# Kernel tuning notes

Measured on AMD Instinct MI355X. Metric: run time of the kernel, lower is better.

The kernel has to match this reference:

```python
import jax, jax.numpy as jnp
import numpy as np

B, S, H, L, NH, FF, V, T = 32, 512, 768, 6, 12, 3072, 30522, 7
DH = H // NH


def setup_inputs():
    key = jax.random.key(0)
    ks = iter(jax.random.split(key, 32))

    def w(shape, scale=0.02):
        return jax.random.normal(next(ks), shape, jnp.float32) * scale

    inp = {
        "word_emb": w((V, H)),
        "pos_emb": w((S, H)),
        "emb_ln_s": jnp.ones((H,), jnp.float32),
        "emb_ln_b": jnp.zeros((H,), jnp.float32),
        "attn_qw": w((L, H, H)), "attn_qb": jnp.zeros((L, H), jnp.float32),
        "attn_kw": w((L, H, H)), "attn_kb": jnp.zeros((L, H), jnp.float32),
        "attn_vw": w((L, H, H)), "attn_vb": jnp.zeros((L, H), jnp.float32),
        "attn_ow": w((L, H, H)), "attn_ob": jnp.zeros((L, H), jnp.float32),
        "ln1_s": jnp.ones((L, H), jnp.float32), "ln1_b": jnp.zeros((L, H), jnp.float32),
        "ffn_w1": w((L, H, FF)), "ffn_b1": jnp.zeros((L, FF), jnp.float32),
        "ffn_w2": w((L, FF, H)), "ffn_b2": jnp.zeros((L, H), jnp.float32),
        "ln2_s": jnp.ones((L, H), jnp.float32), "ln2_b": jnp.zeros((L, H), jnp.float32),
        "cls_w": w((H, T)), "cls_b": jnp.zeros((T,), jnp.float32),
        "crf_start": w((T,), 0.1), "crf_end": w((T,), 0.1), "crf_trans": w((T, T), 0.1),
    }
    lengths = jax.random.randint(next(ks), (B,), S // 2, S + 1)
    attention_mask = (jnp.arange(S)[None, :] < lengths[:, None]).astype(jnp.int32)
    raw_labels = jax.random.randint(next(ks), (B, S), 0, T)
    inp["input_ids"] = jax.random.randint(next(ks), (B, S), 0, V)
    inp["attention_mask"] = attention_mask
    inp["labels"] = jnp.where(attention_mask == 1, raw_labels, -100)  # -100 = ignore
    return inp


def _layer_norm(x, s, b, eps=1e-12):
    m = x.mean(-1, keepdims=True)
    v = ((x - m) ** 2).mean(-1, keepdims=True)
    return (x - m) / jnp.sqrt(v + eps) * s + b


def _forward(params, input_ids, attention_mask, labels):
    (word_emb, pos_emb, emb_ln_s, emb_ln_b, attn_qw, attn_qb, attn_kw, attn_kb,
     attn_vw, attn_vb, attn_ow, attn_ob, ln1_s, ln1_b, ffn_w1, ffn_b1, ffn_w2,
     ffn_b2, ln2_s, ln2_b, cls_w, cls_b, crf_start, crf_end, crf_trans) = params
    amask = attention_mask.astype(bool)            # [B,S]
    # DistilBERT embeddings (word + position, then LayerNorm; dropout = identity in eval)
    x = word_emb[input_ids] + pos_emb[None, :, :]  # [B,S,H]
    x = _layer_norm(x, emb_ln_s, emb_ln_b)
    neg = jnp.finfo(x.dtype).min
    for i in range(L):  # 6 structurally distinct transformer layers
        q = (x @ attn_qw[i] + attn_qb[i]).reshape(B, S, NH, DH).transpose(0, 2, 1, 3)
        k = (x @ attn_kw[i] + attn_kb[i]).reshape(B, S, NH, DH).transpose(0, 2, 1, 3)
        v = (x @ attn_vw[i] + attn_vb[i]).reshape(B, S, NH, DH).transpose(0, 2, 1, 3)
        scores = jnp.einsum('bhqd,bhkd->bhqk', q, k) / jnp.sqrt(jnp.float32(DH))
        scores = jnp.where(amask[:, None, None, :], scores, neg)
        probs = jax.nn.softmax(scores, axis=-1)
        ctx = jnp.einsum('bhqk,bhkd->bhqd', probs, v).transpose(0, 2, 1, 3).reshape(B, S, H)
        x = _layer_norm(x + ctx @ attn_ow[i] + attn_ob[i], ln1_s[i], ln1_b[i])
        h = jax.nn.gelu(x @ ffn_w1[i] + ffn_b1[i], approximate=False)
        x = _layer_norm(x + h @ ffn_w2[i] + ffn_b2[i], ln2_s[i], ln2_b[i])
    emissions = x @ cls_w + cls_b                  # [B,S,T]

    # ---- CRF negative mean log-likelihood (torchcrf semantics, batch_first) ----
    mask = (labels != -100).at[:, 0].set(True)     # [B,S] bool
    safe = jnp.where(mask, labels, 0)
    safe = safe.at[:, 0].set(jnp.clip(safe[:, 0], 0, T - 1))
    b_idx = jnp.arange(B)
    # numerator: score of the given tag sequence
    emit = jnp.take_along_axis(emissions, safe[:, :, None], axis=2)[:, :, 0]  # [B,S]
    trans = crf_trans[safe[:, :-1], safe[:, 1:]]                              # [B,S-1]
    num = crf_start[safe[:, 0]] + emit[:, 0]
    num = num + jnp.sum(jnp.where(mask[:, 1:], trans + emit[:, 1:], 0.0), axis=1)
    seq_ends = mask.sum(axis=1) - 1
    num = num + crf_end[safe[b_idx, seq_ends]]
    # denominator: forward algorithm (logsumexp recursion over timesteps)
    alpha0 = crf_start[None, :] + emissions[:, 0]  # [B,T]

    def step(alpha, xs):
        em_t, m_t = xs                              # [B,T], [B]
        nxt = jax.nn.logsumexp(alpha[:, :, None] + crf_trans[None] + em_t[:, None, :], axis=1)
        return jnp.where(m_t[:, None], nxt, alpha), None

    alpha, _ = jax.lax.scan(step, alpha0,
                            (emissions[:, 1:].transpose(1, 0, 2), mask[:, 1:].T))
    denom = jax.nn.logsumexp(alpha + crf_end[None, :], axis=1)
    return -(num - denom).mean()  # reduction='mean', returned negated


def reference(word_emb, pos_emb, emb_ln_s, emb_ln_b, attn_qw, attn_qb, attn_kw,
              attn_kb, attn_vw, attn_vb, attn_ow, attn_ob, ln1_s, ln1_b, ffn_w1,
              ffn_b1, ffn_w2, ffn_b2, ln2_s, ln2_b, cls_w, cls_b, crf_start,
              crf_end, crf_trans, input_ids, attention_mask, labels):
    params = (word_emb, pos_emb, emb_ln_s, emb_ln_b, attn_qw, attn_qb, attn_kw,
              attn_kb, attn_vw, attn_vb, attn_ow, attn_ob, ln1_s, ln1_b, ffn_w1,
              ffn_b1, ffn_w2, ffn_b2, ln2_s, ln2_b, cls_w, cls_b, crf_start,
              crf_end, crf_trans)
    return _forward(params, input_ids, attention_mask, labels)
```

## Files before the change

kernel.cpp:

```cpp
#include <hip/hip_runtime.h>

constexpr int cB = 32, cS = 512, cH = 768, cL = 6, cNH = 12, cFF = 3072, cT = 7;
constexpr int cM = cB * cS;
constexpr int cDH = cH / cNH;
constexpr int cQS = 2304;

#define DEVI __device__ __forceinline__

typedef __attribute__((ext_vector_type(8))) short bh8_t;
typedef __attribute__((ext_vector_type(4))) float f4_t;
typedef __attribute__((ext_vector_type(4))) unsigned short us4_t;

DEVI unsigned short f2bf(float f) {
  unsigned int u = __float_as_uint(f);
  return (unsigned short)((u + 0x7fffu + ((u >> 16) & 1u)) >> 16);
}
DEVI float bf2f(unsigned short h) { return __uint_as_float(((unsigned int)h) << 16); }

DEVI float fast_erff(float x) {
  const float a = fabsf(x);
  const float t = 1.0f / (1.0f + 0.3275911f * a);
  const float y = 1.0f - (((((1.061405429f * t - 1.453152027f) * t) + 1.421413741f) * t
                            - 0.284496736f) * t + 0.254829592f) * t * __expf(-a * a);
  return copysignf(y, x);
}

typedef __attribute__((address_space(1))) void* gas_t;
typedef __attribute__((address_space(3))) void* las_t;
DEVI void async16(void* lds, const void* g) {
  __builtin_amdgcn_global_load_lds((gas_t)g, (las_t)lds, 16, 0, 0);
}

struct WtransArgs { const float* src[6]; };

__global__ void wtrans_all(WtransArgs args, unsigned short* __restrict__ out) {
  const int m = blockIdx.z;
  const int K = (m == 5) ? cFF : cH;
  const int N = (m == 4) ? cFF : cH;
  int n0, k0;
  if (m < 4) {
    if (blockIdx.x >= 24) return;
    n0 = blockIdx.x * 32; k0 = blockIdx.y * 32;
  } else if (m == 4) {
    n0 = blockIdx.x * 32; k0 = blockIdx.y * 32;
  } else {
    k0 = blockIdx.x * 32; n0 = blockIdx.y * 32;
  }
  const int woffs[6] = {0, 589824, 1179648, 1769472, 2359296, 4718592};
  const float* in = args.src[m];
  unsigned short* o = out + woffs[m];
  __shared__ float tile[32][33];
  const int tx = threadIdx.x, ty = threadIdx.y;
#pragma unroll
  for (int i = 0; i < 4; i++)
    tile[ty + i * 8][tx] = in[(size_t)(k0 + ty + i * 8) * N + n0 + tx];
  __syncthreads();
#pragma unroll
  for (int i = 0; i < 4; i++)
    o[(size_t)(n0 + ty + i * 8) * K + k0 + tx] = f2bf(tile[tx][ty + i * 8]);
}

__global__ void concat_bias(const float* __restrict__ qb, const float* __restrict__ kb,
                            const float* __restrict__ vb, float* __restrict__ out) {
  const int c = blockIdx.x * 256 + threadIdx.x;
  if (c < cQS)
    out[c] = c < cH ? qb[c] : (c < 2 * cH ? kb[c - cH] : vb[c - 2 * cH]);
}

template <bool RESID, bool GELU, bool OUTB>
__global__ __launch_bounds__(256) void gemm_bf16(
    const unsigned short* __restrict__ A, const unsigned short* __restrict__ Bt,
    const float* __restrict__ bias, const float* resid,
    float* outf, unsigned short* __restrict__ outb, int N, int K) {
  __shared__ __align__(16) unsigned short As[128 * 32];
  __shared__ __align__(16) unsigned short Bs[128 * 32];
  const int tid = threadIdx.x;
  const int lane = tid & 63;
  const int wave = tid >> 6;
  const int wm = wave >> 1, wn = wave & 1;
  const int quad = lane >> 4, col = lane & 15;
  const int m0 = blockIdx.y * 128;
  const int n0 = blockIdx.x * 128;

  f4_t acc[4][4] = {};

  const int rA = tid >> 2;
  const int cXor = ((tid & 3) ^ ((tid >> 3) & 3)) << 3;
  const unsigned short* gA = A + (size_t)(m0 + rA) * K + cXor;
  const unsigned short* gB = Bt + (size_t)(n0 + rA) * K + cXor;
  unsigned short* lA0 = As + wave * 512;
  unsigned short* lA1 = As + 2048 + wave * 512;
  unsigned short* lB0 = Bs + wave * 512;
  unsigned short* lB1 = Bs + 2048 + wave * 512;

  const int physq = quad ^ ((col >> 1) & 3);
  const unsigned short* fA[4];
  const unsigned short* fB[4];
#pragma unroll
  for (int t = 0; t < 4; t++) {
    fA[t] = As + (size_t)(wm * 64 + t * 16 + col) * 32 + physq * 8;
    fB[t] = Bs + (size_t)(wn * 64 + t * 16 + col) * 32 + physq * 8;
  }

  for (int k0 = 0; k0 < K; k0 += 32) {
    async16(lA0, gA + k0);
    async16(lA1, gA + (size_t)64 * K + k0);
    async16(lB0, gB + k0);
    async16(lB1, gB + (size_t)64 * K + k0);
    __syncthreads();
    bh8_t af[4], bf[4];
#pragma unroll
    for (int t = 0; t < 4; t++) af[t] = *(const bh8_t*)fA[t];
#pragma unroll
    for (int t = 0; t < 4; t++) bf[t] = *(const bh8_t*)fB[t];
#pragma unroll
    for (int mi = 0; mi < 4; mi++)
#pragma unroll
      for (int ni = 0; ni < 4; ni++)
        acc[mi][ni] = __builtin_amdgcn_mfma_f32_16x16x32_bf16(bf[ni], af[mi],
                                                              acc[mi][ni], 0, 0, 0);
    __syncthreads();
  }

#pragma unroll
  for (int mi = 0; mi < 4; mi++) {
    const size_t rowbase = (size_t)(m0 + wm * 64 + mi * 16 + col) * N;
#pragma unroll
    for (int ni = 0; ni < 4; ni++) {
      const int cb = n0 + wn * 64 + ni * 16 + quad * 4;
      f4_t v = acc[mi][ni] + *(const f4_t*)(bias + cb);
      if (RESID) v += *(const f4_t*)(resid + rowbase + cb);
      if (GELU) {
#pragma unroll
        for (int r = 0; r < 4; r++)
          v[r] = 0.5f * v[r] * (1.0f + fast_erff(v[r] * 0.70710678118654752f));
      }
      if (OUTB) {
        us4_t u;
#pragma unroll
        for (int r = 0; r < 4; r++) u[r] = f2bf(v[r]);
        *(us4_t*)(outb + rowbase + cb) = u;
      } else {
        *(f4_t*)(outf + rowbase + cb) = v;
      }
    }
  }
}

__global__ __launch_bounds__(256) void embed_ln(
    const int* __restrict__ ids, const float* __restrict__ wemb,
    const float* __restrict__ pemb, const float* __restrict__ g,
    const float* __restrict__ be, float* __restrict__ xo,
    unsigned short* __restrict__ xbo) {
  const int token = blockIdx.x;
  const int tid = threadIdx.x;
  const int id = ids[token];
  const int pos = token & (cS - 1);
  const float* wr = wemb + (size_t)id * cH;
  const float* pr = pemb + (size_t)pos * cH;
  float v[3];
#pragma unroll
  for (int i = 0; i < 3; i++) v[i] = wr[tid + i * 256] + pr[tid + i * 256];
  float s = v[0] + v[1] + v[2];
  float s2 = v[0] * v[0] + v[1] * v[1] + v[2] * v[2];
#pragma unroll
  for (int off = 32; off; off >>= 1) { s += __shfl_xor(s, off); s2 += __shfl_xor(s2, off); }
  __shared__ float sa[4], sb[4];
  if ((tid & 63) == 0) { sa[tid >> 6] = s; sb[tid >> 6] = s2; }
  __syncthreads();
  s = sa[0] + sa[1] + sa[2] + sa[3];
  s2 = sb[0] + sb[1] + sb[2] + sb[3];
  const float mean = s * (1.0f / cH);
  const float rstd = rsqrtf(s2 * (1.0f / cH) - mean * mean + 1e-12f);
  float* xr = xo + (size_t)token * cH;
  unsigned short* xbr = xbo + (size_t)token * cH;
#pragma unroll
  for (int i = 0; i < 3; i++) {
    const int c = tid + i * 256;
    const float nv = (v[i] - mean) * rstd * g[c] + be[c];
    xr[c] = nv;
    xbr[c] = f2bf(nv);
  }
}

__global__ __launch_bounds__(256) void ln_fused(
    float* __restrict__ x, const float* __restrict__ g,
    const float* __restrict__ be, unsigned short* __restrict__ xbo) {
  const int token = blockIdx.x;
  const int tid = threadIdx.x;
  float* row = x + (size_t)token * cH;
  float v[3];
#pragma unroll
  for (int i = 0; i < 3; i++) v[i] = row[tid + i * 256];
  float s = v[0] + v[1] + v[2];
  float s2 = v[0] * v[0] + v[1] * v[1] + v[2] * v[2];
#pragma unroll
  for (int off = 32; off; off >>= 1) { s += __shfl_xor(s, off); s2 += __shfl_xor(s2, off); }
  __shared__ float sa[4], sb[4];
  if ((tid & 63) == 0) { sa[tid >> 6] = s; sb[tid >> 6] = s2; }
  __syncthreads();
  s = sa[0] + sa[1] + sa[2] + sa[3];
  s2 = sb[0] + sb[1] + sb[2] + sb[3];
  const float mean = s * (1.0f / cH);
  const float rstd = rsqrtf(s2 * (1.0f / cH) - mean * mean + 1e-12f);
  unsigned short* xbr = xbo + (size_t)token * cH;
#pragma unroll
  for (int i = 0; i < 3; i++) {
    const int c = tid + i * 256;
    const float nv = (v[i] - mean) * rstd * g[c] + be[c];
    row[c] = nv;
    xbr[c] = f2bf(nv);
  }
}

__global__ __launch_bounds__(256, 2) void attn_mfma(
    const unsigned short* __restrict__ qkv, const int* __restrict__ amask,
    unsigned short* __restrict__ ctxb) {
  __shared__ __align__(16) unsigned short Ks[128 * 64];
  __shared__ __align__(16) unsigned short Vt[64 * 128];
  __shared__ __align__(16) unsigned short Ps[4 * 32 * 136];
  __shared__ int lensh[4];

  const int tid = threadIdx.x, lane = tid & 63, wave = tid >> 6;
  const int quad = lane >> 4, col = lane & 15;
  const int wg = blockIdx.x;
  const int qb = wg & 3, h = (wg >> 2) % cNH, b = wg / (4 * cNH);
  const int q0 = qb * 128 + wave * 32;

  const unsigned short* qg = qkv;
  const unsigned short* kg = qkv + cH;
  const unsigned short* vg = qkv + 2 * cH;

  const int* mrow = amask + b * cS;
  int c = mrow[tid] + mrow[tid + 256];
#pragma unroll
  for (int off = 32; off; off >>= 1) c += __shfl_xor(c, off);
  if (lane == 0) lensh[wave] = c;
  __syncthreads();
  const int len = lensh[0] + lensh[1] + lensh[2] + lensh[3];

  const unsigned short* qbase = qg + (size_t)(b * cS + q0) * cQS + h * cDH;
  bh8_t qf[2][2];
#pragma unroll
  for (int mi = 0; mi < 2; mi++)
#pragma unroll
    for (int ks = 0; ks < 2; ks++)
      qf[mi][ks] = *(const bh8_t*)(qbase + (size_t)(mi * 16 + col) * cQS + ks * 32 + quad * 8);

  float mr[2][4], lr[2][4];
  f4_t o[2][4] = {};
#pragma unroll
  for (int mi = 0; mi < 2; mi++)
#pragma unroll
    for (int r = 0; r < 4; r++) { mr[mi][r] = -3.0e38f; lr[mi][r] = 0.0f; }

  unsigned short* Pw = Ps + wave * (32 * 136);

  for (int k0 = 0; k0 < cS; k0 += 128) {
    if (k0 >= len) break;
    __syncthreads();
    const unsigned short* kb = kg + (size_t)(b * cS + k0) * cQS + h * cDH;
    const unsigned short* vb = vg + (size_t)(b * cS + k0) * cQS + h * cDH;
#pragma unroll
    for (int i = 0; i < 4; i++) {
      const int chunk = i * 256 + tid;
      const int key = chunk >> 3;
      const int ld = (chunk & 7) ^ (key & 7);
      async16(Ks + (size_t)(i * 256 + wave * 64) * 8, kb + (size_t)key * cQS + ld * 8);
    }
#pragma unroll
    for (int i = 0; i < 4; i++) {
      const int chunk = i * 256 + tid;
      const int key = chunk >> 3;
      const int ld = chunk & 7;
      const int bk = key >> 3;
      bh8_t vv = *(const bh8_t*)(vb + (size_t)key * cQS + ld * 8);
      unsigned short vs[8];
      *(bh8_t*)vs = vv;
#pragma unroll
      for (int j = 0; j < 8; j++) {
        const int d = ld * 8 + j;
        const int pb = bk ^ j ^ ld;
        Vt[d * 128 + pb * 8 + (key & 7)] = vs[j];
      }
    }
    __syncthreads();

    f4_t s[2][8];
#pragma unroll
    for (int mi = 0; mi < 2; mi++)
#pragma unroll
      for (int n = 0; n < 8; n++) s[mi][n] = f4_t{0.f, 0.f, 0.f, 0.f};
#pragma unroll
    for (int n = 0; n < 8; n++) {
      const int r = n * 16 + col;
#pragma unroll
      for (int ks = 0; ks < 2; ks++) {
        const int phys = (ks * 4 + quad) ^ (col & 7);
        bh8_t kf = *(const bh8_t*)(Ks + (size_t)r * 64 + phys * 8);
        s[0][n] = __builtin_amdgcn_mfma_f32_16x16x32_bf16(qf[0][ks], kf, s[0][n], 0, 0, 0);
        s[1][n] = __builtin_amdgcn_mfma_f32_16x16x32_bf16(qf[1][ks], kf, s[1][n], 0, 0, 0);
      }
    }
#pragma unroll
    for (int n = 0; n < 8; n++) {
      const bool valid = (k0 + n * 16 + col) < len;
#pragma unroll
      for (int mi = 0; mi < 2; mi++)
#pragma unroll
        for (int r = 0; r < 4; r++)
          s[mi][n][r] = valid ? s[mi][n][r] * 0.125f : -3.0e38f;
    }
#pragma unroll
    for (int mi = 0; mi < 2; mi++)
#pragma unroll
      for (int r = 0; r < 4; r++) {
        float v = s[mi][0][r];
#pragma unroll
        for (int n = 1; n < 8; n++) v = fmaxf(v, s[mi][n][r]);
#pragma unroll
        for (int off = 1; off < 16; off <<= 1) v = fmaxf(v, __shfl_xor(v, off));
        const float nm = fmaxf(mr[mi][r], v);
        const float alpha = __expf(mr[mi][r] - nm);
        float rs = 0.0f;
#pragma unroll
        for (int n = 0; n < 8; n++) {
          const float p = __expf(s[mi][n][r] - nm);
          s[mi][n][r] = p;
          rs += p;
        }
#pragma unroll
        for (int off = 1; off < 16; off <<= 1) rs += __shfl_xor(rs, off);
        lr[mi][r] = lr[mi][r] * alpha + rs;
        mr[mi][r] = nm;
#pragma unroll
        for (int nd = 0; nd < 4; nd++) o[mi][nd][r] *= alpha;
      }
#pragma unroll
    for (int mi = 0; mi < 2; mi++)
#pragma unroll
      for (int n = 0; n < 8; n++)
#pragma unroll
        for (int r = 0; r < 4; r++)
          Pw[(mi * 16 + quad * 4 + r) * 136 + n * 16 + col] = f2bf(s[mi][n][r]);
    __syncthreads();
#pragma unroll
    for (int ks = 0; ks < 4; ks++) {
      bh8_t pf[2];
#pragma unroll
      for (int mi = 0; mi < 2; mi++)
        pf[mi] = *(const bh8_t*)(Pw + (size_t)(mi * 16 + col) * 136 + ks * 32 + quad * 8);
#pragma unroll
      for (int nd = 0; nd < 4; nd++) {
        const int d = nd * 16 + col;
        const int pb = (ks * 4 + quad) ^ (d & 7) ^ (d >> 3);
        bh8_t vf = *(const bh8_t*)(Vt + (size_t)d * 128 + pb * 8);
        o[0][nd] = __builtin_amdgcn_mfma_f32_16x16x32_bf16(pf[0], vf, o[0][nd], 0, 0, 0);
        o[1][nd] = __builtin_amdgcn_mfma_f32_16x16x32_bf16(pf[1], vf, o[1][nd], 0, 0, 0);
      }
    }
  }

#pragma unroll
  for (int mi = 0; mi < 2; mi++)
#pragma unroll
    for (int r = 0; r < 4; r++) {
      const float inv = 1.0f / lr[mi][r];
      const int q = q0 + mi * 16 + quad * 4 + r;
      unsigned short* orow = ctxb + (size_t)(b * cS + q) * cH + h * cDH;
#pragma unroll
      for (int nd = 0; nd < 4; nd++) orow[nd * 16 + col] = f2bf(o[mi][nd][r] * inv);
    }
}

__global__ __launch_bounds__(256) void cls_head(
    const float* __restrict__ x, const float* __restrict__ w,
    const float* __restrict__ cb, float* __restrict__ em) {
  const int token = blockIdx.x * 4 + (threadIdx.x >> 6);
  const int lane = threadIdx.x & 63;
  const float* xr = x + (size_t)token * cH;
  float p[cT] = {};
  for (int k = lane; k < cH; k += 64) {
    const float xv = xr[k];
    const float* wr = w + k * cT;
#pragma unroll
    for (int t = 0; t < cT; t++) p[t] += xv * wr[t];
  }
#pragma unroll
  for (int t = 0; t < cT; t++) {
    float r = p[t];
#pragma unroll
    for (int off = 32; off; off >>= 1) r += __shfl_xor(r, off);
    if (lane == t) em[(size_t)token * cT + t] = r + cb[t];
  }
}

__global__ __launch_bounds__(1024) void crf(
    const float* __restrict__ em, const int* __restrict__ labels,
    const float* __restrict__ cstart, const float* __restrict__ cend,
    const float* __restrict__ ctrans, float* __restrict__ out) {
  const int b = blockIdx.x;
  const int tid = threadIdx.x;
  const int wave = tid >> 6, lane = tid & 63;
  const int* lab = labels + b * cS;
  const float* eb = em + (size_t)b * cS * cT;

  __shared__ float mats[16][49];
  __shared__ float mbuf[8][49];
  __shared__ int slen;
  __shared__ float snum;
  if (tid == 0) { slen = 0; snum = 0.0f; }
  __syncthreads();

  if (tid < cS) {
    const int valid = (tid == 0) || (lab[tid] != -100);
    const unsigned long long bal = __ballot(valid);
    if (lane == 0) atomicAdd(&slen, __popcll(bal));
  }
  __syncthreads();
  const int len = slen;

  {
    float np = 0.0f;
    if (tid >= 1 && tid < len)
      np = ctrans[lab[tid - 1] * cT + lab[tid]] + eb[tid * cT + lab[tid]];
#pragma unroll
    for (int off = 32; off; off >>= 1) np += __shfl_xor(np, off);
    if (lane == 0) atomicAdd(&snum, np);
  }

  const int ii = (lane < 49) ? lane / 7 : 0;
  const int jj = (lane < 49) ? lane % 7 : 0;
  const int i7 = ii * 7;
  float trk[cT];
#pragma unroll
  for (int k = 0; k < cT; k++) trk[k] = ctrans[k * cT + jj];

  float Nij = (ii == jj) ? 0.0f : -1.0e30f;
  const int s_beg = 1 + 32 * wave;
  const int s_end = min(s_beg + 32, len);
  for (int s = s_beg; s < s_end; s++) {
    const float ej = eb[s * cT + jj];
    float v[cT];
#pragma unroll
    for (int k = 0; k < cT; k++) v[k] = __shfl(Nij, i7 + k) + trk[k];
    float mx = v[0];
#pragma unroll
    for (int k = 1; k < cT; k++) mx = fmaxf(mx, v[k]);
    float ss = 0.0f;
#pragma unroll
    for (int k = 0; k < cT; k++) ss += __expf(v[k] - mx);
    Nij = mx + __logf(ss) + ej;
  }
  if (lane < 49) mats[wave][lane] = Nij;
  __syncthreads();

  auto compose = [&](const float* Am, const float* Bm) -> float {
    float v[cT];
#pragma unroll
    for (int k = 0; k < cT; k++) v[k] = Am[i7 + k] + Bm[k * 7 + jj];
    float mx = v[0];
#pragma unroll
    for (int k = 1; k < cT; k++) mx = fmaxf(mx, v[k]);
    float ss = 0.0f;
#pragma unroll
    for (int k = 0; k < cT; k++) ss += __expf(v[k] - mx);
    return mx + __logf(ss);
  };
  if (wave < 8 && lane < 49) mbuf[wave][lane] = compose(mats[2 * wave], mats[2 * wave + 1]);
  __syncthreads();
  if (wave < 4 && lane < 49) mats[wave][lane] = compose(mbuf[2 * wave], mbuf[2 * wave + 1]);
  __syncthreads();
  if (wave < 2 && lane < 49) mbuf[wave][lane] = compose(mats[2 * wave], mats[2 * wave + 1]);
  __syncthreads();

  if (wave == 0) {
    float Mij = compose(mbuf[0], mbuf[1]);
    const float a0 = cstart[ii] + eb[ii];
    const float t = a0 + Mij;
    float av[cT];
#pragma unroll
    for (int k = 0; k < cT; k++) av[k] = __shfl(t, k * 7 + lane);
    float mx = av[0];
#pragma unroll
    for (int k = 1; k < cT; k++) mx = fmaxf(mx, av[k]);
    float ss = 0.0f;
#pragma unroll
    for (int k = 0; k < cT; k++) ss += __expf(av[k] - mx);
    const float afin = mx + __logf(ss) + ((lane < cT) ? cend[lane] : 0.0f);
    float dv[cT];
#pragma unroll
    for (int k = 0; k < cT; k++) dv[k] = __shfl(afin, k);
    float dmx = dv[0];
#pragma unroll
    for (int k = 1; k < cT; k++) dmx = fmaxf(dmx, dv[k]);
    float dss = 0.0f;
#pragma unroll
    for (int k = 0; k < cT; k++) dss += __expf(dv[k] - dmx);
    const float denom = dmx + __logf(dss);
    if (lane == 0) {
      const int l0 = lab[0];
      const float num = snum + cstart[l0] + eb[l0] + cend[lab[len - 1]];
      atomicAdd(out, (denom - num) * (1.0f / cB));
    }
  }
}

extern "C" void kernel_launch(void* const* d_in, const int* in_sizes, int n_in,
                              void* d_out, int out_size, void* d_ws, size_t ws_size,
                              hipStream_t stream) {
  const float* word_emb = (const float*)d_in[0];
  const float* pos_emb = (const float*)d_in[1];
  const float* emb_ln_s = (const float*)d_in[2];
  const float* emb_ln_b = (const float*)d_in[3];
  const float* attn_qw = (const float*)d_in[4];
  const float* attn_qb = (const float*)d_in[5];
  const float* attn_kw = (const float*)d_in[6];
  const float* attn_kb = (const float*)d_in[7];
  const float* attn_vw = (const float*)d_in[8];
  const float* attn_vb = (const float*)d_in[9];
  const float* attn_ow = (const float*)d_in[10];
  const float* attn_ob = (const float*)d_in[11];
  const float* ln1_s = (const float*)d_in[12];
  const float* ln1_b = (const float*)d_in[13];
  const float* ffn_w1 = (const float*)d_in[14];
  const float* ffn_b1 = (const float*)d_in[15];
  const float* ffn_w2 = (const float*)d_in[16];
  const float* ffn_b2 = (const float*)d_in[17];
  const float* ln2_s = (const float*)d_in[18];
  const float* ln2_b = (const float*)d_in[19];
  const float* cls_w = (const float*)d_in[20];
  const float* cls_b = (const float*)d_in[21];
  const float* crf_start = (const float*)d_in[22];
  const float* crf_end = (const float*)d_in[23];
  const float* crf_trans = (const float*)d_in[24];
  const int* input_ids = (const int*)d_in[25];
  const int* amask = (const int*)d_in[26];
  const int* labels = (const int*)d_in[27];

  char* ws = (char*)d_ws;
  size_t off = 0;
  auto alloc = [&](size_t bytes) -> void* {
    void* p = ws + off;
    off += (bytes + 255) & ~(size_t)255;
    return p;
  };
  constexpr size_t LW = 7077888;
  unsigned short* Wt = (unsigned short*)alloc(LW * 2);
  float* qkvb = (float*)alloc(cQS * 4);
  float* x = (float*)alloc((size_t)cM * cH * 4);
  unsigned short* xb = (unsigned short*)alloc((size_t)cM * cH * 2);
  unsigned short* un = (unsigned short*)alloc((size_t)cM * cFF * 2);
  unsigned short* qkv = un;
  unsigned short* ctx = un + (size_t)cM * cQS;
  unsigned short* hb = un;
  float* emis = (float*)alloc((size_t)cM * cT * 4);

  hipMemsetAsync(d_out, 0, sizeof(float) * out_size, stream);

  embed_ln<<<cM, 256, 0, stream>>>(input_ids, word_emb, pos_emb, emb_ln_s, emb_ln_b, x, xb);

  for (int i = 0; i < cL; i++) {
    WtransArgs wa;
    wa.src[0] = attn_qw + (size_t)i * cH * cH;
    wa.src[1] = attn_kw + (size_t)i * cH * cH;
    wa.src[2] = attn_vw + (size_t)i * cH * cH;
    wa.src[3] = attn_ow + (size_t)i * cH * cH;
    wa.src[4] = ffn_w1 + (size_t)i * cH * cFF;
    wa.src[5] = ffn_w2 + (size_t)i * cFF * cH;
    wtrans_all<<<dim3(96, 24, 6), dim3(32, 8), 0, stream>>>(wa, Wt);
    concat_bias<<<9, 256, 0, stream>>>(attn_qb + i * cH, attn_kb + i * cH,
                                       attn_vb + i * cH, qkvb);

    gemm_bf16<false, false, true><<<dim3(cQS / 128, cM / 128), 256, 0, stream>>>(
        xb, Wt, qkvb, nullptr, nullptr, qkv, cQS, cH);
    attn_mfma<<<cB * cNH * 4, 256, 0, stream>>>(qkv, amask, ctx);
    gemm_bf16<true, false, false><<<dim3(cH / 128, cM / 128), 256, 0, stream>>>(
        ctx, Wt + 1769472, attn_ob + i * cH, x, x, nullptr, cH, cH);
    ln_fused<<<cM, 256, 0, stream>>>(x, ln1_s + i * cH, ln1_b + i * cH, xb);
    gemm_bf16<false, true, true><<<dim3(cFF / 128, cM / 128), 256, 0, stream>>>(
        xb, Wt + 2359296, ffn_b1 + i * cFF, nullptr, nullptr, hb, cFF, cH);
    gemm_bf16<true, false, false><<<dim3(cH / 128, cM / 128), 256, 0, stream>>>(
        hb, Wt + 4718592, ffn_b2 + i * cH, x, x, nullptr, cH, cFF);
    ln_fused<<<cM, 256, 0, stream>>>(x, ln2_s + i * cH, ln2_b + i * cH, xb);
  }

  cls_head<<<cM / 4, 256, 0, stream>>>(x, cls_w, cls_b, emis);
  crf<<<cB, 1024, 0, stream>>>(emis, labels, crf_start, crf_end, crf_trans, (float*)d_out);
}
```

Before: 3.649 ms.

## Replace 128x128 GEMM with 256x256 tile, 8-wave pipelined bf16 MFMA kernel

Replaces the simple 128x128, 4-wave GEMM, which has one barrier pair per 32-wide K step, with a 256x256 tile, 8-wave kernel. The new kernel uses 64-wide K tiles double-buffered in 128KB of LDS, with async global-to-LDS staging interleaved between MFMA clusters, explicit vmcnt/lgkmcnt waits and s_setprio around MFMA bursts. The goal is to raise arithmetic intensity per tile and overlap memory loads with matrix-core work. The cost is fewer blocks per GEMM, for example only 3x64 blocks for the N=768 GEMMs. It also brings heavy LDS use that may limit occupancy and hand-tuned wait counts that are fragile.

```diff
diff --git a/kernel.cpp b/kernel.cpp
--- a/kernel.cpp
+++ b/kernel.cpp
@@ -67,66 +67,168 @@
     out[c] = c < cH ? qb[c] : (c < 2 * cH ? kb[c - cH] : vb[c - 2 * cH]);
 }
 
+
+DEVI void stage_half(unsigned short* half_lds, const unsigned short* g0, int K, int tid) {
+#pragma unroll
+  for (int j = 0; j < 2; ++j) {
+    const int cid = j * 512 + tid;
+    const int row = cid >> 3;
+    const int sc = (cid & 7) ^ (row & 7);
+    async16(half_lds + (size_t)(j * 512 + (tid & ~63)) * 8,
+            g0 + (size_t)row * K + sc * 8);
+  }
+}
+
+DEVI void load_a4(bh8_t (&dst)[4][2], const unsigned short* base, const int pq[2]) {
+#pragma unroll
+  for (int mi = 0; mi < 4; ++mi)
+#pragma unroll
+    for (int ks = 0; ks < 2; ++ks)
+      dst[mi][ks] = *(const bh8_t*)(base + mi * 1024 + pq[ks]);
+}
+
+DEVI void load_b2(bh8_t (&dst)[2][2], const unsigned short* base, const int pq[2]) {
+#pragma unroll
+  for (int ni = 0; ni < 2; ++ni)
+#pragma unroll
+    for (int ks = 0; ks < 2; ++ks)
+      dst[ni][ks] = *(const bh8_t*)(base + ni * 1024 + pq[ks]);
+}
+
+template <int NI0, int MI0>
+DEVI void qmfma(f4_t (&acc)[8][4], const bh8_t (&bset)[2][2], const bh8_t (&af)[4][2]) {
+#pragma unroll
+  for (int mi = 0; mi < 4; ++mi)
+#pragma unroll
+    for (int ks = 0; ks < 2; ++ks) {
+      acc[MI0 + mi][NI0] = __builtin_amdgcn_mfma_f32_16x16x32_bf16(
+          bset[0][ks], af[mi][ks], acc[MI0 + mi][NI0], 0, 0, 0);
+      acc[MI0 + mi][NI0 + 1] = __builtin_amdgcn_mfma_f32_16x16x32_bf16(
+          bset[1][ks], af[mi][ks], acc[MI0 + mi][NI0 + 1], 0, 0, 0);
+    }
+}
+
+DEVI void wgbar() {
+  asm volatile("" ::: "memory");
+  __builtin_amdgcn_s_barrier();
+  asm volatile("" ::: "memory");
+}
+
 template <bool RESID, bool GELU, bool OUTB>
-__global__ __launch_bounds__(256) void gemm_bf16(
+__global__ __launch_bounds__(512, 2) void gemm256(
     const unsigned short* __restrict__ A, const unsigned short* __restrict__ Bt,
     const float* __restrict__ bias, const float* resid,
     float* outf, unsigned short* __restrict__ outb, int N, int K) {
-  __shared__ __align__(16) unsigned short As[128 * 32];
-  __shared__ __align__(16) unsigned short Bs[128 * 32];
+  __shared__ __align__(16) unsigned short lds[65536];
   const int tid = threadIdx.x;
-  const int lane = tid & 63;
-  const int wave = tid >> 6;
-  const int wm = wave >> 1, wn = wave & 1;
+  const int lane = tid & 63, wave = tid >> 6;
+  const int wm = wave >> 2, wn = wave & 3;
   const int quad = lane >> 4, col = lane & 15;
-  const int m0 = blockIdx.y * 128;
-  const int n0 = blockIdx.x * 128;
-
-  f4_t acc[4][4] = {};
-
-  const int rA = tid >> 2;
-  const int cXor = ((tid & 3) ^ ((tid >> 3) & 3)) << 3;
-  const unsigned short* gA = A + (size_t)(m0 + rA) * K + cXor;
-  const unsigned short* gB = Bt + (size_t)(n0 + rA) * K + cXor;
-  unsigned short* lA0 = As + wave * 512;
-  unsigned short* lA1 = As + 2048 + wave * 512;
-  unsigned short* lB0 = Bs + wave * 512;
-  unsigned short* lB1 = Bs + 2048 + wave * 512;
-
-  const int physq = quad ^ ((col >> 1) & 3);
-  const unsigned short* fA[4];
-  const unsigned short* fB[4];
-#pragma unroll
-  for (int t = 0; t < 4; t++) {
-    fA[t] = As + (size_t)(wm * 64 + t * 16 + col) * 32 + physq * 8;
-    fB[t] = Bs + (size_t)(wn * 64 + t * 16 + col) * 32 + physq * 8;
-  }
-
-  for (int k0 = 0; k0 < K; k0 += 32) {
-    async16(lA0, gA + k0);
-    async16(lA1, gA + (size_t)64 * K + k0);
-    async16(lB0, gB + k0);
-    async16(lB1, gB + (size_t)64 * K + k0);
-    __syncthreads();
-    bh8_t af[4], bf[4];
-#pragma unroll
-    for (int t = 0; t < 4; t++) af[t] = *(const bh8_t*)fA[t];
-#pragma unroll
-    for (int t = 0; t < 4; t++) bf[t] = *(const bh8_t*)fB[t];
-#pragma unroll
-    for (int mi = 0; mi < 4; mi++)
-#pragma unroll
-      for (int ni = 0; ni < 4; ni++)
-        acc[mi][ni] = __builtin_amdgcn_mfma_f32_16x16x32_bf16(bf[ni], af[mi],
-                                                              acc[mi][ni], 0, 0, 0);
-    __syncthreads();
-  }
-
-#pragma unroll
-  for (int mi = 0; mi < 4; mi++) {
-    const size_t rowbase = (size_t)(m0 + wm * 64 + mi * 16 + col) * N;
-#pragma unroll
-    for (int ni = 0; ni < 4; ni++) {
+  const int m0 = blockIdx.y * 256, n0 = blockIdx.x * 256;
+  const int nt = K >> 6;
+
+  const unsigned short* Ag = A + (size_t)m0 * K;
+  const unsigned short* Bg = Bt + (size_t)n0 * K;
+
+  const int aoff = wm * 8192 + col * 64;
+  const int boff = 16384 + (wn >> 1) * 8192 + (wn & 1) * 4096 + col * 64;
+  const int pq[2] = {(quad ^ (col & 7)) * 8, ((quad + 4) ^ (col & 7)) * 8};
+
+  f4_t acc[8][4] = {};
+  bh8_t af[4][2], blo[2][2], bhi[2][2];
+
+  stage_half(lds + 16384, Bg, K, tid);
+  stage_half(lds + 16384 + 8192, Bg + (size_t)128 * K, K, tid);
+  stage_half(lds + 0, Ag, K, tid);
+  stage_half(lds + 8192, Ag + (size_t)128 * K, K, tid);
+  stage_half(lds + 49152, Bg + 64, K, tid);
+  stage_half(lds + 49152 + 8192, Bg + (size_t)128 * K + 64, K, tid);
+
+  for (int t = 0; t < nt; t += 2) {
+    const bool tail = (t + 2 >= nt);
+    const size_t k1 = (size_t)(t + 1) << 6;
+    const size_t k2 = (size_t)(t + 2) << 6;
+    const size_t k3 = (size_t)(t + 3) << 6;
+
+    stage_half(lds + 32768, Ag + k1, K, tid);
+    asm volatile("s_waitcnt vmcnt(6)" ::: "memory");
+    wgbar();
+    load_b2(blo, lds + boff, pq);
+    load_a4(af, lds + aoff, pq);
+    asm volatile("s_waitcnt lgkmcnt(0)" ::: "memory");
+    __builtin_amdgcn_s_setprio(1);
+    qmfma<0, 0>(acc, blo, af);
+    __builtin_amdgcn_s_setprio(0);
+    wgbar();
+
+    load_b2(bhi, lds + boff + 2048, pq);
+    stage_half(lds + 32768 + 8192, Ag + (size_t)128 * K + k1, K, tid);
+    wgbar();
+    asm volatile("s_waitcnt lgkmcnt(0)" ::: "memory");
+    __builtin_amdgcn_s_setprio(1);
+    qmfma<2, 0>(acc, bhi, af);
+    __builtin_amdgcn_s_setprio(0);
+    wgbar();
+
+    load_a4(af, lds + aoff + 4096, pq);
+    if (!tail) stage_half(lds + 16384, Bg + k2, K, tid);
+    wgbar();
+    asm volatile("s_waitcnt lgkmcnt(0)" ::: "memory");
+    __builtin_amdgcn_s_setprio(1);
+    qmfma<0, 4>(acc, blo, af);
+    __builtin_amdgcn_s_setprio(0);
+    wgbar();
+
+    if (!tail) stage_half(lds + 16384 + 8192, Bg + (size_t)128 * K + k2, K, tid);
+    wgbar();
+    __builtin_amdgcn_s_setprio(1);
+    qmfma<2, 4>(acc, bhi, af);
+    __builtin_amdgcn_s_setprio(0);
+    wgbar();
+
+    if (!tail) stage_half(lds + 0, Ag + k2, K, tid);
+    if (tail) { asm volatile("s_waitcnt vmcnt(0)" ::: "memory"); }
+    else      { asm volatile("s_waitcnt vmcnt(6)" ::: "memory"); }
+    wgbar();
+    load_b2(blo, lds + 32768 + boff, pq);
+    load_a4(af, lds + 32768 + aoff, pq);
+    asm volatile("s_waitcnt lgkmcnt(0)" ::: "memory");
+    __builtin_amdgcn_s_setprio(1);
+    qmfma<0, 0>(acc, blo, af);
+    __builtin_amdgcn_s_setprio(0);
+    wgbar();
+
+    load_b2(bhi, lds + 32768 + boff + 2048, pq);
+    if (!tail) stage_half(lds + 8192, Ag + (size_t)128 * K + k2, K, tid);
+    wgbar();
+    asm volatile("s_waitcnt lgkmcnt(0)" ::: "memory");
+    __builtin_amdgcn_s_setprio(1);
+    qmfma<2, 0>(acc, bhi, af);
+    __builtin_amdgcn_s_setprio(0);
+    wgbar();
+
+    load_a4(af, lds + 32768 + aoff + 4096, pq);
+    if (!tail) stage_half(lds + 49152, Bg + k3, K, tid);
+    wgbar();
+    asm volatile("s_waitcnt lgkmcnt(0)" ::: "memory");
+    __builtin_amdgcn_s_setprio(1);
+    qmfma<0, 4>(acc, blo, af);
+    __builtin_amdgcn_s_setprio(0);
+    wgbar();
+
+    if (!tail) stage_half(lds + 49152 + 8192, Bg + (size_t)128 * K + k3, K, tid);
+    wgbar();
+    __builtin_amdgcn_s_setprio(1);
+    qmfma<2, 4>(acc, bhi, af);
+    __builtin_amdgcn_s_setprio(0);
+    wgbar();
+  }
+
+#pragma unroll
+  for (int mi = 0; mi < 8; ++mi) {
+    const size_t rowbase = (size_t)(m0 + wm * 128 + mi * 16 + col) * N;
+#pragma unroll
+    for (int ni = 0; ni < 4; ++ni) {
       const int cb = n0 + wn * 64 + ni * 16 + quad * 4;
       f4_t v = acc[mi][ni] + *(const f4_t*)(bias + cb);
       if (RESID) v += *(const f4_t*)(resid + rowbase + cb);
@@ -572,15 +674,15 @@
     concat_bias<<<9, 256, 0, stream>>>(attn_qb + i * cH, attn_kb + i * cH,
                                        attn_vb + i * cH, qkvb);
 
-    gemm_bf16<false, false, true><<<dim3(cQS / 128, cM / 128), 256, 0, stream>>>(
+    gemm256<false, false, true><<<dim3(cQS / 256, cM / 256), 512, 0, stream>>>(
         xb, Wt, qkvb, nullptr, nullptr, qkv, cQS, cH);
     attn_mfma<<<cB * cNH * 4, 256, 0, stream>>>(qkv, amask, ctx);
-    gemm_bf16<true, false, false><<<dim3(cH / 128, cM / 128), 256, 0, stream>>>(
+    gemm256<true, false, false><<<dim3(cH / 256, cM / 256), 512, 0, stream>>>(
         ctx, Wt + 1769472, attn_ob + i * cH, x, x, nullptr, cH, cH);
     ln_fused<<<cM, 256, 0, stream>>>(x, ln1_s + i * cH, ln1_b + i * cH, xb);
-    gemm_bf16<false, true, true><<<dim3(cFF / 128, cM / 128), 256, 0, stream>>>(
+    gemm256<false, true, true><<<dim3(cFF / 256, cM / 256), 512, 0, stream>>>(
         xb, Wt + 2359296, ffn_b1 + i * cFF, nullptr, nullptr, hb, cFF, cH);
-    gemm_bf16<true, false, false><<<dim3(cH / 128, cM / 128), 256, 0, stream>>>(
+    gemm256<true, false, false><<<dim3(cH / 256, cM / 256), 512, 0, stream>>>(
         hb, Wt + 4718592, ffn_b2 + i * cH, x, x, nullptr, cH, cFF);
     ln_fused<<<cM, 256, 0, stream>>>(x, ln2_s + i * cH, ln2_b + i * cH, xb);
   }
```

New measurement: 3.074 ms. 1.19x faster.

## Replace 128x128 GEMM with 256x256 double-buffered, grid-swizzled 512-thread kernel

Applied to the files above, without the earlier changes.

Replaces the 128x128-tile, 256-thread bf16 GEMM with a 256x256-tile, 512-thread kernel. The new kernel double-buffers A and B in LDS with explicit vmcnt waits, splits each k-step into two MFMA halves, raises wave priority around the MFMAs, and remaps block IDs in an XCD-style swizzle. The aims are more data reuse per tile, loads that overlap compute, and better L2 locality. In exchange it needs 64KB of LDS per block and 128 accumulator registers per thread, and its fragile hand-written waitcnt logic risks low occupancy or races.

```diff
diff --git a/kernel.cpp b/kernel.cpp
--- a/kernel.cpp
+++ b/kernel.cpp
@@ -67,66 +67,96 @@
     out[c] = c < cH ? qb[c] : (c < 2 * cH ? kb[c - cH] : vb[c - 2 * cH]);
 }
 
+
+DEVI void stage32(unsigned short* buf, const unsigned short* g0, int K, int tid) {
+  const int d = (tid & ~63) << 3;
+  async16(buf + d, g0);
+  async16(buf + 4096 + d, g0 + (size_t)128 * K);
+}
+
+DEVI void wgbar() {
+  asm volatile("" ::: "memory");
+  __builtin_amdgcn_s_barrier();
+  asm volatile("" ::: "memory");
+}
+
 template <bool RESID, bool GELU, bool OUTB>
-__global__ __launch_bounds__(256) void gemm_bf16(
+__global__ __launch_bounds__(512, 4) void gemm256(
     const unsigned short* __restrict__ A, const unsigned short* __restrict__ Bt,
     const float* __restrict__ bias, const float* resid,
     float* outf, unsigned short* __restrict__ outb, int N, int K) {
-  __shared__ __align__(16) unsigned short As[128 * 32];
-  __shared__ __align__(16) unsigned short Bs[128 * 32];
+  __shared__ __align__(16) unsigned short lds[32768];
   const int tid = threadIdx.x;
-  const int lane = tid & 63;
-  const int wave = tid >> 6;
-  const int wm = wave >> 1, wn = wave & 1;
+  const int lane = tid & 63, wave = tid >> 6;
+  const int wm = wave >> 2, wn = wave & 3;
   const int quad = lane >> 4, col = lane & 15;
-  const int m0 = blockIdx.y * 128;
-  const int n0 = blockIdx.x * 128;
-
-  f4_t acc[4][4] = {};
-
-  const int rA = tid >> 2;
-  const int cXor = ((tid & 3) ^ ((tid >> 3) & 3)) << 3;
-  const unsigned short* gA = A + (size_t)(m0 + rA) * K + cXor;
-  const unsigned short* gB = Bt + (size_t)(n0 + rA) * K + cXor;
-  unsigned short* lA0 = As + wave * 512;
-  unsigned short* lA1 = As + 2048 + wave * 512;
-  unsigned short* lB0 = Bs + wave * 512;
-  unsigned short* lB1 = Bs + 2048 + wave * 512;
-
-  const int physq = quad ^ ((col >> 1) & 3);
-  const unsigned short* fA[4];
-  const unsigned short* fB[4];
-#pragma unroll
-  for (int t = 0; t < 4; t++) {
-    fA[t] = As + (size_t)(wm * 64 + t * 16 + col) * 32 + physq * 8;
-    fB[t] = Bs + (size_t)(wn * 64 + t * 16 + col) * 32 + physq * 8;
-  }
-
-  for (int k0 = 0; k0 < K; k0 += 32) {
-    async16(lA0, gA + k0);
-    async16(lA1, gA + (size_t)64 * K + k0);
-    async16(lB0, gB + k0);
-    async16(lB1, gB + (size_t)64 * K + k0);
-    __syncthreads();
-    bh8_t af[4], bf[4];
-#pragma unroll
-    for (int t = 0; t < 4; t++) af[t] = *(const bh8_t*)fA[t];
-#pragma unroll
-    for (int t = 0; t < 4; t++) bf[t] = *(const bh8_t*)fB[t];
-#pragma unroll
-    for (int mi = 0; mi < 4; mi++)
-#pragma unroll
-      for (int ni = 0; ni < 4; ni++)
-        acc[mi][ni] = __builtin_amdgcn_mfma_f32_16x16x32_bf16(bf[ni], af[mi],
+  const int nt = K >> 5;
+
+  const int nx = gridDim.x;
+  const int nwg = nx * gridDim.y;
+  int lid = blockIdx.y * nx + blockIdx.x;
+  lid = (lid & 7) * (nwg >> 3) + (lid >> 3);
+  const int m0 = (lid / nx) * 256, n0 = (lid % nx) * 256;
+
+  const int srow = tid >> 2;
+  const int soff = srow * K + (((tid & 3) ^ ((srow >> 1) & 3)) << 3);
+  const unsigned short* Agp = A + (size_t)m0 * K + soff;
+  const unsigned short* Bgp = Bt + (size_t)n0 * K + soff;
+
+  const int paq = (quad ^ ((col >> 1) & 3)) << 3;
+  const int aoff = wm * 4096 + col * 32 + paq;
+  const int boff = wn * 2048 + col * 32 + paq;
+
+  f4_t acc[8][4] = {};
+  bh8_t a4[4], b4[4];
+
+  stage32(lds + 0, Agp, K, tid);
+  stage32(lds + 8192, Bgp, K, tid);
+  stage32(lds + 24576, Bgp + 32, K, tid);
+
+  for (int t = 0; t < nt; ++t) {
+    const int p = t & 1;
+    unsigned short* Ab = lds + p * 16384;
+    unsigned short* Bb = Ab + 8192;
+
+    if (t < nt - 1) { asm volatile("s_waitcnt vmcnt(2)" ::: "memory"); }
+    else            { asm volatile("s_waitcnt vmcnt(0)" ::: "memory"); }
+    wgbar();
+    if (t + 1 < nt) stage32(lds + (1 - p) * 16384, Agp + ((size_t)(t + 1) << 5), K, tid);
+#pragma unroll
+    for (int mi = 0; mi < 4; ++mi) a4[mi] = *(const bh8_t*)(Ab + aoff + mi * 512);
+#pragma unroll
+    for (int ni = 0; ni < 4; ++ni) b4[ni] = *(const bh8_t*)(Bb + boff + ni * 512);
+    asm volatile("s_waitcnt lgkmcnt(0)" ::: "memory");
+    __builtin_amdgcn_s_setprio(1);
+#pragma unroll
+    for (int mi = 0; mi < 4; ++mi)
+#pragma unroll
+      for (int ni = 0; ni < 4; ++ni)
+        acc[mi][ni] = __builtin_amdgcn_mfma_f32_16x16x32_bf16(b4[ni], a4[mi],
                                                               acc[mi][ni], 0, 0, 0);
-    __syncthreads();
-  }
-
-#pragma unroll
-  for (int mi = 0; mi < 4; mi++) {
-    const size_t rowbase = (size_t)(m0 + wm * 64 + mi * 16 + col) * N;
-#pragma unroll
-    for (int ni = 0; ni < 4; ni++) {
+    __builtin_amdgcn_s_setprio(0);
+
+    wgbar();
+    if (t + 2 < nt) stage32(Bb, Bgp + ((size_t)(t + 2) << 5), K, tid);
+#pragma unroll
+    for (int mi = 0; mi < 4; ++mi) a4[mi] = *(const bh8_t*)(Ab + aoff + (mi + 4) * 512);
+    asm volatile("s_waitcnt lgkmcnt(0)" ::: "memory");
+    __builtin_amdgcn_s_setprio(1);
+#pragma unroll
+    for (int mi = 0; mi < 4; ++mi)
+#pragma unroll
+      for (int ni = 0; ni < 4; ++ni)
+        acc[mi + 4][ni] = __builtin_amdgcn_mfma_f32_16x16x32_bf16(b4[ni], a4[mi],
+                                                                  acc[mi + 4][ni], 0, 0, 0);
+    __builtin_amdgcn_s_setprio(0);
+  }
+
+#pragma unroll
+  for (int mi = 0; mi < 8; ++mi) {
+    const size_t rowbase = (size_t)(m0 + wm * 128 + mi * 16 + col) * N;
+#pragma unroll
+    for (int ni = 0; ni < 4; ++ni) {
       const int cb = n0 + wn * 64 + ni * 16 + quad * 4;
       f4_t v = acc[mi][ni] + *(const f4_t*)(bias + cb);
       if (RESID) v += *(const f4_t*)(resid + rowbase + cb);
@@ -572,15 +602,15 @@
     concat_bias<<<9, 256, 0, stream>>>(attn_qb + i * cH, attn_kb + i * cH,
                                        attn_vb + i * cH, qkvb);
 
-    gemm_bf16<false, false, true><<<dim3(cQS / 128, cM / 128), 256, 0, stream>>>(
+    gemm256<false, false, true><<<dim3(cQS / 256, cM / 256), 512, 0, stream>>>(
         xb, Wt, qkvb, nullptr, nullptr, qkv, cQS, cH);
     attn_mfma<<<cB * cNH * 4, 256, 0, stream>>>(qkv, amask, ctx);
-    gemm_bf16<true, false, false><<<dim3(cH / 128, cM / 128), 256, 0, stream>>>(
+    gemm256<true, false, false><<<dim3(cH / 256, cM / 256), 512, 0, stream>>>(
         ctx, Wt + 1769472, attn_ob + i * cH, x, x, nullptr, cH, cH);
     ln_fused<<<cM, 256, 0, stream>>>(x, ln1_s + i * cH, ln1_b + i * cH, xb);
-    gemm_bf16<false, true, true><<<dim3(cFF / 128, cM / 128), 256, 0, stream>>>(
+    gemm256<false, true, true><<<dim3(cFF / 256, cM / 256), 512, 0, stream>>>(
         xb, Wt + 2359296, ffn_b1 + i * cFF, nullptr, nullptr, hb, cFF, cH);
-    gemm_bf16<true, false, false><<<dim3(cH / 128, cM / 128), 256, 0, stream>>>(
+    gemm256<true, false, false><<<dim3(cH / 256, cM / 256), 512, 0, stream>>>(
         hb, Wt + 4718592, ffn_b2 + i * cH, x, x, nullptr, cH, cFF);
     ln_fused<<<cM, 256, 0, stream>>>(x, ln2_s + i * cH, ln2_b + i * cH, xb);
   }
```

New measurement: 14.26 ms. 3.91x slower.
